# Kernel tuning notes

Hardware: AMD Instinct MI355X
Metric: run time of the kernel (lower is better)

Reference implementation:

```python
import jax, jax.numpy as jnp
import numpy as np

N_NODES = 100000
N_EDGES = 3200000
D_FEAT = 256
TOP_K = 50000


def setup_inputs() -> dict:
    key = jax.random.key(0)
    k1, k2, k3 = jax.random.split(key, 3)
    h = jax.random.normal(k1, (N_NODES, D_FEAT), dtype=jnp.float32)
    W = jax.random.normal(k2, (D_FEAT, 1), dtype=jnp.float32) * (1.0 / np.sqrt(D_FEAT))
    b = jnp.zeros((1,), dtype=jnp.float32)
    edge_index = jax.random.randint(k3, (2, N_EDGES), 0, N_NODES, dtype=jnp.int64)
    return {"h": h, "W": W, "b": b, "edge_index": edge_index, "top_k": TOP_K}


def reference(h, W, b, edge_index, top_k):
    # scores = sigmoid(Linear(h)) -> [N, 1]
    scores = jax.nn.sigmoid(h @ W + b)  # [N, 1]
    # top-k node selection by score (descending), like dgl.topk_nodes
    top_scores, node_ids = jax.lax.top_k(scores[:, 0], top_k)  # [k], [k]
    # gather features of selected nodes, scale by their scores
    new_h = h[node_ids] * top_scores[:, None]  # [k, d]
    # induced-subgraph edges: edge kept iff both endpoints selected
    member = jnp.zeros((h.shape[0],), dtype=bool).at[node_ids].set(True)
    edge_mask = member[edge_index[0]] & member[edge_index[1]]  # [E]
    return new_h, node_ids, edge_mask
```

## Files before the change

### kernel.cpp

```cpp
#include <hip/hip_runtime.h>
#include <math.h>

#define N_NODES 100000
#define D_FEAT  256
#define TOP_K   50000
#define NBINS   65536
#define NCHUNK  64
#define CUTPOS  (N_NODES - TOP_K)
#define ROWSTRIDE 260
#define NBITW   3200
#define FUSE_GRID   2048
#define EMIT_BLOCKS 1408

typedef float  fx4 __attribute__((ext_vector_type(4)));
typedef float  fx2 __attribute__((ext_vector_type(2)));


__device__ __forceinline__ int bucket_of(float s) {
    int b = (int)(s * 65536.0f);
    return min(max(b, 0), NBINS - 1);
}

__device__ __forceinline__ float np_expf(float x) {
    float q  = rintf(x * 1.44269504088896341f);
    float xr = fmaf(-q, 0.693359375f, x);
    xr       = fmaf(-q, -2.12194440e-4f, xr);
    float x2 = xr * xr;
    float p  = 1.9875691500E-4f;
    p = fmaf(p, xr, 1.3981999507E-3f);
    p = fmaf(p, xr, 8.3334519073E-3f);
    p = fmaf(p, xr, 4.1665795894E-2f);
    p = fmaf(p, xr, 1.6666665459E-1f);
    p = fmaf(p, xr, 5.0000001201E-1f);
    p = fmaf(p, x2, xr);
    p = p + 1.0f;
    return ldexpf(p, (int)q);
}

__global__ void score_kernel(const float* __restrict__ h,
                             const float* __restrict__ W,
                             const float* __restrict__ bvec,
                             float* __restrict__ s32,
                             int* __restrict__ hist) {
    __shared__ float rows[32 * ROWSTRIDE];
    __shared__ float wl[256];
    int tid  = threadIdx.x;
    int wave = tid >> 6;
    int lane = tid & 63;
    int g    = lane >> 3;
    int l    = lane & 7;

    wl[tid] = W[tid];

    int nodeBase = blockIdx.x * 32 + wave * 8;
#pragma unroll
    for (int r = 0; r < 8; ++r) {
        float4 v = ((const float4*)(h + (size_t)(nodeBase + r) * D_FEAT))[lane];
        *((float4*)&rows[(wave * 8 + r) * ROWSTRIDE + lane * 4]) = v;
    }
    __syncthreads();

    float wreg[32];
#pragma unroll
    for (int i = 0; i < 32; ++i) wreg[i] = wl[i * 8 + l];

    const float* myrow = &rows[(wave * 8 + g) * ROWSTRIDE];
    float acc = 0.0f;
#pragma unroll
    for (int i = 0; i < 32; ++i)
        acc = fmaf(myrow[i * 8 + l], wreg[i], acc);

    float b01 = acc + __shfl_xor(acc, 1, 64);
    float b23 = b01 + __shfl_xor(b01, 2, 64);
    float z   = b23 + __shfl_xor(b23, 4, 64);

    z = z + bvec[0];
    float t = np_expf(-z);
    float s = 1.0f / (1.0f + t);

    if (l == 0) {
        int node = nodeBase + g;
        __builtin_nontemporal_store(s, &s32[node]);
        atomicAdd(&hist[bucket_of(s)], 1);
    }
}

__global__ void scan_chunks_kernel(const int* __restrict__ hist,
                                   int* __restrict__ offs,
                                   int* __restrict__ cursor,
                                   int* __restrict__ chunkSum) {
    __shared__ int wsum[4];
    int tid  = threadIdx.x;
    int lane = tid & 63;
    int wid  = tid >> 6;
    int base = blockIdx.x * 1024 + tid * 4;

    int4 hv = *((const int4*)(hist + base));
    int e1 = hv.x;
    int e2 = hv.x + hv.y;
    int e3 = e2 + hv.z;
    int tot = e3 + hv.w;

    int incl = tot;
#pragma unroll
    for (int d = 1; d < 64; d <<= 1) {
        int t = __shfl_up(incl, d, 64);
        if (lane >= d) incl += t;
    }
    if (lane == 63) wsum[wid] = incl;
    __syncthreads();
    int wbase = 0;
#pragma unroll
    for (int w = 0; w < 3; ++w)
        if (w < wid) wbase += wsum[w];

    int excl = wbase + (incl - tot);
    int4 ov = make_int4(excl, excl + e1, excl + e2, excl + e3);
    *((int4*)(offs + base))   = ov;
    *((int4*)(cursor + base)) = ov;
    if (tid == 255) chunkSum[blockIdx.x] = excl + tot;
}

__device__ __forceinline__ void build_base(const int* __restrict__ chunkSum,
                                           int* sbase, int tid) {
    if (tid < 64) {
        int v = chunkSum[tid];
        int inc = v;
#pragma unroll
        for (int d = 1; d < 64; d <<= 1) {
            int t = __shfl_up(inc, d, 64);
            if (tid >= d) inc += t;
        }
        sbase[tid] = inc - v;
    }
}

__global__ void scatter_kernel(const float* __restrict__ s32,
                               int* __restrict__ cursor,
                               const int* __restrict__ offs,
                               const int* __restrict__ chunkSum,
                               unsigned int* __restrict__ bits,
                               float* __restrict__ ss,
                               int* __restrict__ si) {
    __shared__ int sbase[64];
    int tid = threadIdx.x;
    build_base(chunkSum, sbase, tid);
    __syncthreads();
    int i = blockIdx.x * 256 + tid;
    if (i >= N_NODES) return;
    float s = s32[i];
    int b = bucket_of(s);
    int bn = b + 1;
    int gend = (bn == NBINS) ? N_NODES : sbase[bn >> 10] + offs[bn];
    if (gend <= CUTPOS) return;
    int pos = atomicAdd(&cursor[b], 1);
    int gbase = sbase[b >> 10];
    ss[gbase + pos] = s;
    si[gbase + pos] = i;
    if (gbase + offs[b] >= CUTPOS)
        atomicOr(&bits[(unsigned)i >> 5], 1u << (i & 31));
}

__global__ void bucket_sort_kernel(const int* __restrict__ offs,
                                   const int* __restrict__ chunkSum,
                                   unsigned int* __restrict__ bits,
                                   float* __restrict__ ss,
                                   int* __restrict__ si) {
    __shared__ int sbase[64];
    int tid = threadIdx.x;
    build_base(chunkSum, sbase, tid);
    __syncthreads();
    int b = blockIdx.x * 256 + tid;
    int s0 = sbase[b >> 10] + offs[b];
    int e  = (b == NBINS - 1) ? N_NODES : sbase[(b + 1) >> 10] + offs[b + 1];
    if (e <= CUTPOS) return;
    for (int i = s0 + 1; i < e; ++i) {
        float ks = ss[i];
        int   ki = si[i];
        int j = i - 1;
        while (j >= s0) {
            float ps = ss[j];
            int   pi = si[j];
            bool gt = (ps > ks) || (ps == ks && pi < ki);
            if (!gt) break;
            ss[j + 1] = ps;
            si[j + 1] = pi;
            --j;
        }
        ss[j + 1] = ks;
        si[j + 1] = ki;
    }
    if (s0 < CUTPOS) {
        for (int i = CUTPOS; i < e; ++i) {
            int id = si[i];
            atomicOr(&bits[(unsigned)id >> 5], 1u << (id & 31));
        }
    }
}

__device__ __forceinline__ unsigned mem_bit(const unsigned int* __restrict__ bits,
                                            int s) {
    return (bits[(unsigned)s >> 5] >> (s & 31)) & 1u;
}

__global__ void emit_edge_kernel(const float* __restrict__ h,
                                 const float* __restrict__ ss,
                                 const int* __restrict__ si,
                                 const int* __restrict__ ei,
                                 const unsigned int* __restrict__ bits,
                                 float* __restrict__ out_newh,
                                 float* __restrict__ out_ids,
                                 float* __restrict__ out_mask,
                                 int E) {
    int tid = threadIdx.x;
    int bid = blockIdx.x;

    if (bid < EMIT_BLOCKS) {
        int lane = tid & 63;
        int wg   = bid * 4 + (tid >> 6);
        for (int row = wg; row < TOP_K; row += EMIT_BLOCKS * 4) {
            int p = N_NODES - 1 - row;
            int id  = si[p];
            float s = ss[p];
            if (lane == 0) __builtin_nontemporal_store((float)id, &out_ids[row]);
            const float4* hv = (const float4*)(h + (size_t)id * D_FEAT);
            float4 v = hv[lane];
            fx4 o = { v.x * s, v.y * s, v.z * s, v.w * s };
            __builtin_nontemporal_store(
                o, (fx4*)(out_newh + (size_t)row * D_FEAT) + lane);
        }
        return;
    }

    __shared__ int sflag;
    if (tid < 64) {
        int v = ei[2 * tid + 1];
        unsigned long long m = __ballot(v == 0);
        if (tid == 0) sflag = (m == ~0ULL) ? 1 : 0;
    }
    __syncthreads();
    int flag = sflag;

    int npairs = (E + 1) / 2;
    int stride = (FUSE_GRID - EMIT_BLOCKS) * 256;
    for (int k = (bid - EMIT_BLOCKS) * 256 + tid; k < npairs; k += stride) {
        int i0 = 2 * k;
        int i1 = i0 + 1;
        if (i1 < E) {
            int s0, d0, s1, d1;
            if (flag) {
                int4 a  = ((const int4*)ei)[k];
                int4 bq = ((const int4*)(ei + 2 * (size_t)E))[k];
                s0 = a.x;  s1 = a.z;
                d0 = bq.x; d1 = bq.z;
            } else {
                int2 a  = ((const int2*)ei)[k];
                int2 bq = ((const int2*)(ei + (size_t)E))[k];
                s0 = a.x;  s1 = a.y;
                d0 = bq.x; d1 = bq.y;
            }
            bool ok0 = ((unsigned)s0 < (unsigned)N_NODES) &&
                       ((unsigned)d0 < (unsigned)N_NODES) &&
                       mem_bit(bits, s0) && mem_bit(bits, d0);
            bool ok1 = ((unsigned)s1 < (unsigned)N_NODES) &&
                       ((unsigned)d1 < (unsigned)N_NODES) &&
                       mem_bit(bits, s1) && mem_bit(bits, d1);
            fx2 m = { ok0 ? 1.0f : 0.0f, ok1 ? 1.0f : 0.0f };
            __builtin_nontemporal_store(m, (fx2*)out_mask + k);
        } else {
            int s0, d0;
            if (flag) { s0 = ei[2 * i0]; d0 = ei[2 * ((size_t)E + i0)]; }
            else      { s0 = ei[i0];     d0 = ei[(size_t)E + i0]; }
            bool ok0 = ((unsigned)s0 < (unsigned)N_NODES) &&
                       ((unsigned)d0 < (unsigned)N_NODES) &&
                       mem_bit(bits, s0) && mem_bit(bits, d0);
            __builtin_nontemporal_store(ok0 ? 1.0f : 0.0f, &out_mask[i0]);
        }
    }
}

extern "C" void kernel_launch(void* const* d_in, const int* in_sizes, int n_in,
                              void* d_out, int out_size, void* d_ws, size_t ws_size,
                              hipStream_t stream) {
    const float* h  = (const float*)d_in[0];
    const float* W  = (const float*)d_in[1];
    const float* bv = (const float*)d_in[2];
    const int*   ei = (const int*)d_in[3];
    const int E = in_sizes[3] / 2;

    char* ws = (char*)d_ws;
    float*        s32      = (float*)(ws + 0);
    float*        ss       = (float*)(ws + 400000);
    int*          si       = (int*)(ws + 800000);
    int*          hist     = (int*)(ws + 1200000);
    unsigned int* bits     = (unsigned int*)(ws + 1462144);
    int*          offs     = (int*)(ws + 1562144);
    int*          cursor   = (int*)(ws + 1824288);
    int*          chunkSum = (int*)(ws + 2086432);

    float* out      = (float*)d_out;
    float* out_newh = out;
    float* out_ids  = out + (size_t)TOP_K * D_FEAT;
    float* out_mask = out + (size_t)TOP_K * D_FEAT + TOP_K;

    (void)hipMemsetAsync(ws + 1200000, 0, 274944, stream);

    score_kernel<<<N_NODES / 32, 256, 0, stream>>>(h, W, bv, s32, hist);
    scan_chunks_kernel<<<NCHUNK, 256, 0, stream>>>(hist, offs, cursor, chunkSum);
    scatter_kernel<<<(N_NODES + 255) / 256, 256, 0, stream>>>(s32, cursor, offs,
                                                              chunkSum, bits, ss, si);
    bucket_sort_kernel<<<NBINS / 256, 256, 0, stream>>>(offs, chunkSum, bits, ss, si);
    emit_edge_kernel<<<FUSE_GRID, 256, 0, stream>>>(h, ss, si, ei, bits,
                                                    out_newh, out_ids, out_mask, E);
}
```

Baseline: 235.5 us.

## Pack score and index into 64-bit sort keys and shrink histogram bins

Replaces the separate score and index arrays with one 64-bit key (score bits high, inverted index low), so the insertion sort does one load, compare and store per step instead of two loads and a compound comparison. The bucket count drops from 65536 to 16384 with matching chunk counts, which shrinks the histogram, scan and memset. The trade-off is larger buckets and therefore longer per-thread insertion sorts. Fewer sort threads also do useful work, while bin-related memory traffic and launch work go down.

```diff
diff --git a/kernel.cpp b/kernel.cpp
--- a/kernel.cpp
+++ b/kernel.cpp
@@ -4,8 +4,8 @@
 #define N_NODES 100000
 #define D_FEAT  256
 #define TOP_K   50000
-#define NBINS   65536
-#define NCHUNK  64
+#define NBINS   16384
+#define NCHUNK  16
 #define CUTPOS  (N_NODES - TOP_K)
 #define ROWSTRIDE 260
 #define NBITW   3200
@@ -17,7 +17,7 @@
 
 
 __device__ __forceinline__ int bucket_of(float s) {
-    int b = (int)(s * 65536.0f);
+    int b = (int)(s * 16384.0f);
     return min(max(b, 0), NBINS - 1);
 }
 
@@ -123,11 +123,11 @@
 
 __device__ __forceinline__ void build_base(const int* __restrict__ chunkSum,
                                            int* sbase, int tid) {
-    if (tid < 64) {
+    if (tid < NCHUNK) {
         int v = chunkSum[tid];
         int inc = v;
 #pragma unroll
-        for (int d = 1; d < 64; d <<= 1) {
+        for (int d = 1; d < NCHUNK; d <<= 1) {
             int t = __shfl_up(inc, d, 64);
             if (tid >= d) inc += t;
         }
@@ -140,9 +140,8 @@
                                const int* __restrict__ offs,
                                const int* __restrict__ chunkSum,
                                unsigned int* __restrict__ bits,
-                               float* __restrict__ ss,
-                               int* __restrict__ si) {
-    __shared__ int sbase[64];
+                               unsigned long long* __restrict__ sk) {
+    __shared__ int sbase[NCHUNK];
     int tid = threadIdx.x;
     build_base(chunkSum, sbase, tid);
     __syncthreads();
@@ -155,8 +154,9 @@
     if (gend <= CUTPOS) return;
     int pos = atomicAdd(&cursor[b], 1);
     int gbase = sbase[b >> 10];
-    ss[gbase + pos] = s;
-    si[gbase + pos] = i;
+    unsigned long long key =
+        ((unsigned long long)__float_as_uint(s) << 32) | (unsigned)(~i);
+    sk[gbase + pos] = key;
     if (gbase + offs[b] >= CUTPOS)
         atomicOr(&bits[(unsigned)i >> 5], 1u << (i & 31));
 }
@@ -164,9 +164,8 @@
 __global__ void bucket_sort_kernel(const int* __restrict__ offs,
                                    const int* __restrict__ chunkSum,
                                    unsigned int* __restrict__ bits,
-                                   float* __restrict__ ss,
-                                   int* __restrict__ si) {
-    __shared__ int sbase[64];
+                                   unsigned long long* __restrict__ sk) {
+    __shared__ int sbase[NCHUNK];
     int tid = threadIdx.x;
     build_base(chunkSum, sbase, tid);
     __syncthreads();
@@ -175,24 +174,19 @@
     int e  = (b == NBINS - 1) ? N_NODES : sbase[(b + 1) >> 10] + offs[b + 1];
     if (e <= CUTPOS) return;
     for (int i = s0 + 1; i < e; ++i) {
-        float ks = ss[i];
-        int   ki = si[i];
+        unsigned long long k = sk[i];
         int j = i - 1;
         while (j >= s0) {
-            float ps = ss[j];
-            int   pi = si[j];
-            bool gt = (ps > ks) || (ps == ks && pi < ki);
-            if (!gt) break;
-            ss[j + 1] = ps;
-            si[j + 1] = pi;
+            unsigned long long pk = sk[j];
+            if (pk <= k) break;
+            sk[j + 1] = pk;
             --j;
         }
-        ss[j + 1] = ks;
-        si[j + 1] = ki;
+        sk[j + 1] = k;
     }
     if (s0 < CUTPOS) {
         for (int i = CUTPOS; i < e; ++i) {
-            int id = si[i];
+            int id = (int)~(unsigned)sk[i];
             atomicOr(&bits[(unsigned)id >> 5], 1u << (id & 31));
         }
     }
@@ -204,8 +198,7 @@
 }
 
 __global__ void emit_edge_kernel(const float* __restrict__ h,
-                                 const float* __restrict__ ss,
-                                 const int* __restrict__ si,
+                                 const unsigned long long* __restrict__ sk,
                                  const int* __restrict__ ei,
                                  const unsigned int* __restrict__ bits,
                                  float* __restrict__ out_newh,
@@ -220,8 +213,9 @@
         int wg   = bid * 4 + (tid >> 6);
         for (int row = wg; row < TOP_K; row += EMIT_BLOCKS * 4) {
             int p = N_NODES - 1 - row;
-            int id  = si[p];
-            float s = ss[p];
+            unsigned long long key = sk[p];
+            int id  = (int)~(unsigned)key;
+            float s = __uint_as_float((unsigned)(key >> 32));
             if (lane == 0) __builtin_nontemporal_store((float)id, &out_ids[row]);
             const float4* hv = (const float4*)(h + (size_t)id * D_FEAT);
             float4 v = hv[lane];
@@ -289,27 +283,26 @@
     const int E = in_sizes[3] / 2;
 
     char* ws = (char*)d_ws;
-    float*        s32      = (float*)(ws + 0);
-    float*        ss       = (float*)(ws + 400000);
-    int*          si       = (int*)(ws + 800000);
-    int*          hist     = (int*)(ws + 1200000);
-    unsigned int* bits     = (unsigned int*)(ws + 1462144);
-    int*          offs     = (int*)(ws + 1562144);
-    int*          cursor   = (int*)(ws + 1824288);
-    int*          chunkSum = (int*)(ws + 2086432);
+    float*              s32      = (float*)(ws + 0);
+    unsigned long long* sk       = (unsigned long long*)(ws + 400000);
+    int*                hist     = (int*)(ws + 1200000);
+    unsigned int*       bits     = (unsigned int*)(ws + 1265536);
+    int*                offs     = (int*)(ws + 1278336);
+    int*                cursor   = (int*)(ws + 1343872);
+    int*                chunkSum = (int*)(ws + 1409408);
 
     float* out      = (float*)d_out;
     float* out_newh = out;
     float* out_ids  = out + (size_t)TOP_K * D_FEAT;
     float* out_mask = out + (size_t)TOP_K * D_FEAT + TOP_K;
 
-    (void)hipMemsetAsync(ws + 1200000, 0, 274944, stream);
+    (void)hipMemsetAsync(ws + 1200000, 0, 78336, stream);
 
     score_kernel<<<N_NODES / 32, 256, 0, stream>>>(h, W, bv, s32, hist);
     scan_chunks_kernel<<<NCHUNK, 256, 0, stream>>>(hist, offs, cursor, chunkSum);
     scatter_kernel<<<(N_NODES + 255) / 256, 256, 0, stream>>>(s32, cursor, offs,
-                                                              chunkSum, bits, ss, si);
-    bucket_sort_kernel<<<NBINS / 256, 256, 0, stream>>>(offs, chunkSum, bits, ss, si);
-    emit_edge_kernel<<<FUSE_GRID, 256, 0, stream>>>(h, ss, si, ei, bits,
+                                                              chunkSum, bits, sk);
+    bucket_sort_kernel<<<NBINS / 256, 256, 0, stream>>>(offs, chunkSum, bits, sk);
+    emit_edge_kernel<<<FUSE_GRID, 256, 0, stream>>>(h, sk, ei, bits,
                                                     out_newh, out_ids, out_mask, E);
 }
```

Result: slower. 262.2 us (+11.4%).
